# Kernel optimization log

Measured on AMD Instinct MI355X. Metric: run time of the kernel, lower is better.

## Reference

```python
import jax, jax.numpy as jnp
import numpy as np

B, S, E, H, L, V = 64, 512, 256, 256, 5, 50001  # vocab_size+1 rows, padding_idx=0
GC = 256  # gcn_hidden
NC = [10, 5]


def lstm_dir(x, Wih, Whh, b):
    # x: [B,S,D]; Wih: [4H,D]; Whh: [4H,H]; b: [4H] (= b_ih + b_hh)
    h0 = jnp.zeros((x.shape[0], Whh.shape[1]), x.dtype)
    def step(carry, xt):
        h, c = carry
        g = xt @ Wih.T + h @ Whh.T + b
        i, f, gg, o = jnp.split(g, 4, axis=-1)  # torch gate order i,f,g,o
        c = jax.nn.sigmoid(f) * c + jax.nn.sigmoid(i) * jnp.tanh(gg)
        h = jax.nn.sigmoid(o) * jnp.tanh(c)
        return (h, c), h
    _, hs = jax.lax.scan(step, (h0, h0), jnp.swapaxes(x, 0, 1))
    return jnp.swapaxes(hs, 0, 1)  # [B,S,H]


def layer_norm(x, g, b, eps=1e-5):
    mu = jnp.mean(x, -1, keepdims=True)
    var = jnp.mean((x - mu) ** 2, -1, keepdims=True)
    return (x - mu) * jax.lax.rsqrt(var + eps) * g + b


def banded_adj_matmul(x, mask):
    # adj has only super/sub-diagonal ones, masked by m_i*m_j, row-normalized (+1e-8).
    m = mask
    m_next = jnp.pad(m[:, 1:], ((0, 0), (0, 1)))
    m_prev = jnp.pad(m[:, :-1], ((0, 0), (1, 0)))
    rs = m * (m_prev + m_next) + 1e-8  # row sums
    c_next = (m * m_next / rs)[:, :, None]
    c_prev = (m * m_prev / rs)[:, :, None]
    x_next = jnp.pad(x[:, 1:], ((0, 0), (0, 1), (0, 0)))
    x_prev = jnp.pad(x[:, :-1], ((0, 0), (1, 0), (0, 0)))
    return c_next * x_next + c_prev * x_prev


def gcn_layer(x, mask, W, b, gamma, beta):
    h = banded_adj_matmul(x, mask)
    h = h @ W.T + b
    h = h + x  # in_dim == out_dim -> residual
    return jax.nn.relu(layer_norm(h, gamma, beta))


def setup_inputs() -> dict:
    key = jax.random.key(0)
    ks = jax.random.split(key, 24)
    rn = lambda k, sh, s=0.05: jax.random.normal(k, sh, jnp.float32) * s
    seq = jax.random.randint(ks[0], (B, S), 0, V, jnp.int32)
    mask = jnp.ones((B, S), jnp.float32)
    aux = rn(ks[1], (B, 6), 1.0)
    emb_table = rn(ks[2], (V, E), 0.1).at[0].set(0.0)  # padding_idx=0
    Wih0 = rn(ks[3], (2, 4 * H, E))
    Whh0 = rn(ks[4], (2, 4 * H, H))
    b0 = rn(ks[5], (2, 4 * H))
    Wih = rn(ks[6], (L - 1, 2, 4 * H, 2 * H))
    Whh = rn(ks[7], (L - 1, 2, 4 * H, H))
    bL = rn(ks[8], (L - 1, 2, 4 * H))
    gcn_W = rn(ks[9], (3, GC, E))
    gcn_b = rn(ks[10], (3, GC))
    gcn_gamma = jnp.ones((3, GC), jnp.float32)
    gcn_beta = jnp.zeros((3, GC), jnp.float32)
    fusion = 2 * H + GC + 6
    fc1_W = rn(ks[11], (512, fusion))
    fc1_b = rn(ks[12], (512,))
    fc2_W = rn(ks[13], (256, 512))
    fc2_b = rn(ks[14], (256,))
    head0_W = rn(ks[15], (NC[0], 256))
    head0_b = rn(ks[16], (NC[0],))
    head1_W = rn(ks[17], (NC[1], 256))
    head1_b = rn(ks[18], (NC[1],))
    return dict(seq=seq, mask=mask, aux=aux, emb_table=emb_table, Wih0=Wih0,
                Whh0=Whh0, b0=b0, Wih=Wih, Whh=Whh, bL=bL, gcn_W=gcn_W,
                gcn_b=gcn_b, gcn_gamma=gcn_gamma, gcn_beta=gcn_beta,
                fc1_W=fc1_W, fc1_b=fc1_b, fc2_W=fc2_W, fc2_b=fc2_b,
                head0_W=head0_W, head0_b=head0_b, head1_W=head1_W, head1_b=head1_b)


def reference(seq, mask, aux, emb_table, Wih0, Whh0, b0, Wih, Whh, bL,
              gcn_W, gcn_b, gcn_gamma, gcn_beta, fc1_W, fc1_b, fc2_W, fc2_b,
              head0_W, head0_b, head1_W, head1_b):
    emb = emb_table[seq]  # [B,S,E]; dropout = identity (eval)
    # 5-layer bidirectional LSTM
    out = emb
    for l in range(L):
        wih, whh, b = (Wih0, Whh0, b0) if l == 0 else (Wih[l - 1], Whh[l - 1], bL[l - 1])
        fwd = lstm_dir(out, wih[0], whh[0], b[0])
        bwd = jnp.flip(lstm_dir(jnp.flip(out, 1), wih[1], whh[1], b[1]), 1)
        out = jnp.concatenate([fwd, bwd], -1)  # [B,S,2H]
    lstm_out = out * mask[:, :, None]
    denom = jnp.clip(jnp.sum(mask, 1, keepdims=True), 1e-8)
    lstm_feat = jnp.sum(lstm_out, 1) / denom  # [B,2H]
    # GCN stack over banded adjacency
    g = emb
    for i in range(3):
        g = gcn_layer(g, mask, gcn_W[i], gcn_b[i], gcn_gamma[i], gcn_beta[i])
    g = g * mask[:, :, None]
    gcn_feat = jnp.sum(g, 1) / denom  # [B,GC]
    fused = jnp.concatenate([lstm_feat, gcn_feat, aux], 1)
    s = jax.nn.relu(fused @ fc1_W.T + fc1_b)
    s = jax.nn.relu(s @ fc2_W.T + fc2_b)
    return (s @ head0_W.T + head0_b, s @ head1_W.T + head1_b)
```

## Files before the change

kernel.cpp:

```cpp
#include <hip/hip_runtime.h>
#include <stdint.h>
#include <stddef.h>

typedef __bf16 bf16;
typedef __bf16 bf16x8 __attribute__((ext_vector_type(8)));
typedef __bf16 bf16x4 __attribute__((ext_vector_type(4)));
typedef float  f32x4  __attribute__((ext_vector_type(4)));
typedef int    v4i    __attribute__((ext_vector_type(4)));

#define NB   64
#define NS   512
#define NE   256
#define NH   256
#define NL   5
#define NGC  256
#define FUSION 774

__device__ __forceinline__ float sigm(float x) {
    return __fdividef(1.f, 1.f + __expf(-x));
}
__device__ __forceinline__ float tanh_(float x) {
    return __fdividef(2.f, 1.f + __expf(-2.f * x)) - 1.f;
}

__device__ __forceinline__ void gload_lds16(const void* g, void* l) {
    __builtin_amdgcn_global_load_lds(
        (const __attribute__((address_space(1))) void*)g,
        (__attribute__((address_space(3))) void*)l,
        16, 0, 0);
}

__global__ void k_cvt(const float* __restrict__ src, bf16* __restrict__ dst, int n4) {
    int i = blockIdx.x * 256 + threadIdx.x;
    if (i >= n4) return;
    f32x4 v = ((const f32x4*)src)[i];
    bf16x4 o;
    o[0] = (bf16)v[0]; o[1] = (bf16)v[1]; o[2] = (bf16)v[2]; o[3] = (bf16)v[3];
    ((bf16x4*)dst)[i] = o;
}

__global__ void k_cvt_perm(const float* __restrict__ src, bf16* __restrict__ dst,
                           int K, int nrows) {
    int r = blockIdx.x * 4 + (threadIdx.x >> 6);
    int lane = threadIdx.x & 63;
    if (r >= nrows) return;
    int g = r & 3, j = (r >> 2) & 255;
    int srcrow = (r & ~1023) | (g << 8) | j;
    const float* s = src + (size_t)srcrow * K;
    bf16* dp = dst + (size_t)r * K;
    for (int c = lane * 4; c < K; c += 256) {
        f32x4 v = *(const f32x4*)(s + c);
        bf16x4 o;
        o[0] = (bf16)v[0]; o[1] = (bf16)v[1]; o[2] = (bf16)v[2]; o[3] = (bf16)v[3];
        *(bf16x4*)(dp + c) = o;
    }
}

__global__ void k_perm_bias(const float* __restrict__ b0, const float* __restrict__ bL,
                            float* __restrict__ pb) {
    int i = blockIdx.x * 256 + threadIdx.x;
    int r = i & 2047;
    int layer = i >> 11;
    int g = r & 3, j = (r >> 2) & 255, dh = r >> 10;
    int srcidx = dh * 1024 + g * 256 + j;
    float v = (layer == 0) ? b0[srcidx] : bL[(size_t)(layer - 1) * 2048 + srcidx];
    pb[i] = v;
}

__global__ void k_embed(const int* __restrict__ seq, const float* __restrict__ table,
                        float* __restrict__ ef, bf16* __restrict__ eb) {
    int t  = blockIdx.x * 256 + threadIdx.x;
    int bs = t >> 6;
    int c4 = (t & 63) << 2;
    int row = seq[bs];
    f32x4 v = *(const f32x4*)(table + (size_t)row * NE + c4);
    *(f32x4*)(ef + (size_t)bs * NE + c4) = v;
    bf16x4 o;
    o[0] = (bf16)v[0]; o[1] = (bf16)v[1]; o[2] = (bf16)v[2]; o[3] = (bf16)v[3];
    *(bf16x4*)(eb + (size_t)bs * NE + c4) = o;
}

__global__ __launch_bounds__(256, 2)
void k_gemm(const bf16* __restrict__ A, const bf16* __restrict__ W,
            const float* __restrict__ bias, void* __restrict__ Cout,
            int M, int N, int K, int out_mode) {
    __shared__ __align__(16) bf16 sA[128 * 64];
    __shared__ __align__(16) bf16 sB[128 * 64];
    const int mblk = M >> 7;
    int bm = blockIdx.x % mblk;
    int bn = blockIdx.x / mblk;
    int m0 = bm << 7, n0 = bn << 7;
    int tid  = threadIdx.x;
    int wave = tid >> 6, lane = tid & 63;
    int wm = wave >> 1, wn = wave & 1;
    int l15 = lane & 15, quad = lane >> 4;

    f32x4 acc[4][4] = {};

    const int r0 = tid >> 3;
    const int c0 = (tid & 7) * 8;
    const bf16* Ab = A + (size_t)(m0 + r0) * K + c0;
    const bf16* Wb = W + (size_t)(n0 + r0) * K + c0;
    bf16* sAd = sA + tid * 8;
    bf16* sBd = sB + tid * 8;

    for (int k0 = 0; k0 < K; k0 += 64) {
#pragma unroll
        for (int i = 0; i < 4; i++) {
            gload_lds16(Ab + (size_t)(i * 32) * K + k0, sAd + i * 2048);
            gload_lds16(Wb + (size_t)(i * 32) * K + k0, sBd + i * 2048);
        }
        __syncthreads();
#pragma unroll
        for (int kk = 0; kk < 2; kk++) {
            bf16x8 af[4], bfr[4];
#pragma unroll
            for (int mt = 0; mt < 4; mt++)
                af[mt] = *(const bf16x8*)(sA + (wm * 64 + mt * 16 + l15) * 64 + kk * 32 + quad * 8);
#pragma unroll
            for (int nt = 0; nt < 4; nt++)
                bfr[nt] = *(const bf16x8*)(sB + (wn * 64 + nt * 16 + l15) * 64 + kk * 32 + quad * 8);
#pragma unroll
            for (int mt = 0; mt < 4; mt++)
#pragma unroll
                for (int nt = 0; nt < 4; nt++)
                    acc[mt][nt] = __builtin_amdgcn_mfma_f32_16x16x32_bf16(af[mt], bfr[nt], acc[mt][nt], 0, 0, 0);
        }
        __syncthreads();
    }
#pragma unroll
    for (int mt = 0; mt < 4; mt++) {
#pragma unroll
        for (int nt = 0; nt < 4; nt++) {
            int col = n0 + wn * 64 + nt * 16 + l15;
            float bv = bias[col];
            int row0 = m0 + wm * 64 + mt * 16 + quad * 4;
#pragma unroll
            for (int r4 = 0; r4 < 4; r4++) {
                float v = acc[mt][nt][r4] + bv;
                int r = row0 + r4;
                if (out_mode == 1) {
                    ((bf16*)Cout)[(size_t)r * N + col] = (bf16)v;
                } else {
                    ((float*)Cout)[(size_t)r * N + col] = v;
                }
            }
        }
    }
}

__global__ void k_prep_i8(const float* __restrict__ Whh0, const float* __restrict__ WhhL,
                          signed char* __restrict__ Wp8, float* __restrict__ scales) {
    int gw = blockIdx.x * 4 + (threadIdx.x >> 6);
    int lane = threadIdx.x & 63;
    int row = gw & 1023;
    int d = (gw >> 10) & 1;
    int layer = gw >> 11;
    const float* src = (layer == 0)
        ? (Whh0 + ((size_t)d * 1024 + row) * 256)
        : (WhhL + (((size_t)(layer - 1) * 2 + d) * 1024 + row) * 256);
    f32x4 v = *(const f32x4*)(src + lane * 4);
    float am = fmaxf(fmaxf(fabsf(v[0]), fabsf(v[1])), fmaxf(fabsf(v[2]), fabsf(v[3])));
#pragma unroll
    for (int off = 32; off >= 1; off >>= 1) am = fmaxf(am, __shfl_xor(am, off));
    am = fmaxf(am, 1e-8f);
    float inv = 127.f / am;
    int q0 = (int)__builtin_rintf(v[0] * inv);
    int q1 = (int)__builtin_rintf(v[1] * inv);
    int q2 = (int)__builtin_rintf(v[2] * inv);
    int q3 = (int)__builtin_rintf(v[3] * inv);
    uint32_t packed = (q0 & 255) | ((q1 & 255) << 8) | ((q2 & 255) << 16) | ((q3 & 255) << 24);
    int g = row >> 8, rem = row & 255;
    int w = rem >> 4, l15r = rem & 15;
    int k = lane * 4;
    int kt = k >> 6, q = (k >> 4) & 3, j = k & 15;
    size_t cell = ((size_t)layer * 2 + d) * 256 + (w * 4 + g) * 4 + kt;
    *(uint32_t*)(Wp8 + cell * 1024 + (q * 16 + l15r) * 16 + j) = packed;
    if (lane == 0)
        scales[((size_t)layer * 2 + d) * 1024 + row] = am * (1.f / (127.f * 127.f));
}

__global__ __launch_bounds__(512, 2)
void k_lstm_i8(const bf16* __restrict__ G,
               const signed char* __restrict__ Wp8,
               const float* __restrict__ sc,
               bf16* __restrict__ io_out)
{
    __shared__ signed char hs[2][2 * 4 * 80];

    const int d   = blockIdx.x & 1;
    const int bg  = blockIdx.x >> 1;
    const int tid = threadIdx.x;
    const int w = tid >> 6, lane = tid & 63;
    const int l15 = lane & 15, quad = lane >> 4;
    const int b_loc = quad & 1;
    const int jg    = quad >> 1;
    const int b = bg * 2 + b_loc;
    const int j = (w + jg * 8) * 16 + l15;

    v4i Wr[2][4][4];
#pragma unroll
    for (int sl = 0; sl < 2; sl++) {
        const int ws = w + sl * 8;
        const signed char* wb = Wp8 + ((size_t)d * 256 + ws * 16) * 1024 + lane * 16;
#pragma unroll
        for (int g = 0; g < 4; g++)
#pragma unroll
            for (int kt = 0; kt < 4; kt++)
                Wr[sl][g][kt] = *(const v4i*)(wb + (g * 4 + kt) * 1024);
    }
#pragma unroll
    for (int sl = 0; sl < 2; sl++)
#pragma unroll
        for (int g = 0; g < 4; g++)
#pragma unroll
            for (int kt = 0; kt < 4; kt++)
                asm volatile("" : "+v"(Wr[sl][g][kt]));

    float scv[4];
#pragma unroll
    for (int g = 0; g < 4; g++)
        scv[g] = sc[d * 1024 + g * 256 + j];

    const bf16* gbase = G + d * 1024 + j * 4;
    const size_t iob = (size_t)b * NS * 512 + d * 256 + j;

    const int hwr = (b_loc * 4 + (j >> 6)) * 80 + (j & 63);
    const int hrd = (((l15 >> 2) & 1) * 4 + (l15 & 3)) * 80 + quad * 16;
    const int rr = l15 & 3;

    float cst = 0.f;

    bf16x4 gcur = *(const bf16x4*)(gbase + (size_t)(b * 512 + (d ? (NS - 1) : 0)) * 2048);
    bf16x4 gnxt = *(const bf16x4*)(gbase + (size_t)(b * 512 + (d ? (NS - 2) : 1)) * 2048);

    {
        bf16x4 gfut = *(const bf16x4*)(gbase + (size_t)(b * 512 + (d ? (NS - 3) : 2)) * 2048);
        float pi = (float)gcur[0];
        float pg = (float)gcur[2], po = (float)gcur[3];
        float ig = sigm(pi), gc = tanh_(pg), og = sigm(po);
        float c = ig * gc;
        cst = c;
        float hh = og * tanh_(c);
        const int tcur = d ? (NS - 1) : 0;
        io_out[iob + (size_t)tcur * 512] = (bf16)hh;
        hs[0][hwr] = (signed char)(int)__builtin_rintf(hh * 127.f);
        gcur = gnxt; gnxt = gfut;
        asm volatile("s_waitcnt lgkmcnt(0)" ::: "memory");
        __builtin_amdgcn_s_barrier();
        asm volatile("" ::: "memory");
    }

    for (int t = 1; t < NS; t++) {
        const int rb = (t + 1) & 1, wbuf = t & 1;

        bf16x4 gfut = gcur;
        if (t + 2 < NS) {
            const int tt2 = d ? (NS - 3 - t) : (t + 2);
            gfut = *(const bf16x4*)(gbase + (size_t)(b * 512 + tt2) * 2048);
        }

        v4i acc[2][4] = {};
        {
            v4i chunk = *(const v4i*)&hs[rb][hrd];
            v4i a[4];
#pragma unroll
            for (int kt = 0; kt < 4; kt++) {
                a[kt][0] = (rr == kt) ? chunk[0] : 0;
                a[kt][1] = (rr == kt) ? chunk[1] : 0;
                a[kt][2] = (rr == kt) ? chunk[2] : 0;
                a[kt][3] = (rr == kt) ? chunk[3] : 0;
            }
#pragma unroll
            for (int sl = 0; sl < 2; sl++)
#pragma unroll
                for (int g = 0; g < 4; g++)
#pragma unroll
                    for (int kt = 0; kt < 4; kt++)
                        acc[sl][g] = __builtin_amdgcn_mfma_i32_16x16x64_i8(a[kt], Wr[sl][g][kt], acc[sl][g], 0, 0, 0);
        }

        int s[4];
#pragma unroll
        for (int g = 0; g < 4; g++) {
            int s0 = acc[0][g][0] + acc[0][g][1] + acc[0][g][2] + acc[0][g][3];
            int s1 = acc[1][g][0] + acc[1][g][1] + acc[1][g][2] + acc[1][g][3];
            s[g] = jg ? s1 : s0;
        }
        float pi = (float)s[0] * scv[0] + (float)gcur[0];
        float pf = (float)s[1] * scv[1] + (float)gcur[1];
        float pg = (float)s[2] * scv[2] + (float)gcur[2];
        float po = (float)s[3] * scv[3] + (float)gcur[3];
        float ig = sigm(pi), fg = sigm(pf), gc = tanh_(pg), og = sigm(po);
        float c = fg * cst + ig * gc;
        cst = c;
        float hh = og * tanh_(c);
        const int tcur = d ? (NS - 1 - t) : t;
        io_out[iob + (size_t)tcur * 512] = (bf16)hh;
        hs[wbuf][hwr] = (signed char)(int)__builtin_rintf(hh * 127.f);

        gcur = gnxt; gnxt = gfut;

        asm volatile("s_waitcnt lgkmcnt(0)" ::: "memory");
        __builtin_amdgcn_s_barrier();
        asm volatile("" ::: "memory");
    }
}

__global__ void k_banded(const float* __restrict__ x, const float* __restrict__ mask,
                         bf16* __restrict__ outb) {
    int t  = blockIdx.x * 256 + threadIdx.x;
    int bs = t >> 6;
    int c4 = (t & 63) << 2;
    int s = bs & (NS - 1);
    float m  = mask[bs];
    float mn = (s < NS - 1) ? mask[bs + 1] : 0.f;
    float mp = (s > 0)      ? mask[bs - 1] : 0.f;
    float rs = m * (mp + mn) + 1e-8f;
    float cn = m * mn / rs;
    float cp = m * mp / rs;
    f32x4 vn = {}, vp = {};
    if (s < NS - 1) vn = *(const f32x4*)(x + (size_t)(bs + 1) * NGC + c4);
    if (s > 0)      vp = *(const f32x4*)(x + (size_t)(bs - 1) * NGC + c4);
    bf16x4 o;
#pragma unroll
    for (int i = 0; i < 4; i++) o[i] = (bf16)(cn * vn[i] + cp * vp[i]);
    *(bf16x4*)(outb + (size_t)bs * NGC + c4) = o;
}

__global__ void k_gcnpost(const float* __restrict__ gemm_out, const float* __restrict__ x,
                          const float* __restrict__ gamma, const float* __restrict__ beta,
                          float* __restrict__ outx) {
    int row  = blockIdx.x * 4 + (threadIdx.x >> 6);
    int lane = threadIdx.x & 63;
    const float* h  = gemm_out + (size_t)row * NGC;
    const float* xr = x + (size_t)row * NGC;
    f32x4 hv = *(const f32x4*)(h + lane * 4);
    f32x4 xv = *(const f32x4*)(xr + lane * 4);
    f32x4 v;
#pragma unroll
    for (int i = 0; i < 4; i++) v[i] = hv[i] + xv[i];
    float sum = v[0] + v[1] + v[2] + v[3];
#pragma unroll
    for (int off = 32; off >= 1; off >>= 1) sum += __shfl_xor(sum, off);
    float mu = sum * (1.f / NGC);
    float sq = 0.f;
    f32x4 dv;
#pragma unroll
    for (int i = 0; i < 4; i++) { dv[i] = v[i] - mu; sq += dv[i] * dv[i]; }
#pragma unroll
    for (int off = 32; off >= 1; off >>= 1) sq += __shfl_xor(sq, off);
    float inv = rsqrtf(sq * (1.f / NGC) + 1e-5f);
    f32x4 o;
#pragma unroll
    for (int i = 0; i < 4; i++) {
        int c = lane * 4 + i;
        float y = dv[i] * inv * gamma[c] + beta[c];
        o[i] = fmaxf(y, 0.f);
    }
    *(f32x4*)(outx + (size_t)row * NGC + lane * 4) = o;
}

__global__ void k_pool_bf16(const bf16* __restrict__ src, const float* __restrict__ mask,
                            float* __restrict__ feat) {
    int b = blockIdx.x, f = threadIdx.x;
    float acc = 0.f, dm = 0.f;
    for (int t = 0; t < NS; t++) {
        float m = mask[b * NS + t];
        acc += m * (float)src[((size_t)b * NS + t) * 512 + f];
        dm += m;
    }
    feat[b * 512 + f] = acc / fmaxf(dm, 1e-8f);
}
__global__ void k_pool_f32(const float* __restrict__ src, const float* __restrict__ mask,
                           float* __restrict__ feat) {
    int b = blockIdx.x, f = threadIdx.x;
    float acc = 0.f, dm = 0.f;
    for (int t = 0; t < NS; t++) {
        float m = mask[b * NS + t];
        acc += m * src[((size_t)b * NS + t) * NGC + f];
        dm += m;
    }
    feat[b * NGC + f] = acc / fmaxf(dm, 1e-8f);
}

__global__ __launch_bounds__(512)
void k_head(const float* __restrict__ lfeat, const float* __restrict__ gfeat,
            const float* __restrict__ aux,
            const float* __restrict__ fc1W, const float* __restrict__ fc1b,
            const float* __restrict__ fc2W, const float* __restrict__ fc2b,
            const float* __restrict__ h0W, const float* __restrict__ h0b,
            const float* __restrict__ h1W, const float* __restrict__ h1b,
            float* __restrict__ out) {
    __shared__ float fused[FUSION];
    __shared__ float s1[512];
    __shared__ float s2[256];
    int m = blockIdx.x, tid = threadIdx.x;
    if (tid < 512) fused[tid] = lfeat[m * 512 + tid];
    if (tid < 256) fused[512 + tid] = gfeat[m * 256 + tid];
    if (tid < 6)   fused[768 + tid] = aux[m * 6 + tid];
    __syncthreads();
    {
        float a = fc1b[tid];
        const float* w = fc1W + (size_t)tid * FUSION;
        for (int k = 0; k < FUSION; k++) a += w[k] * fused[k];
        s1[tid] = fmaxf(a, 0.f);
    }
    __syncthreads();
    if (tid < 256) {
        float a = fc2b[tid];
        const float* w = fc2W + (size_t)tid * 512;
        for (int k = 0; k < 512; k++) a += w[k] * s1[k];
        s2[tid] = fmaxf(a, 0.f);
    }
    __syncthreads();
    if (tid < 15) {
        if (tid < 10) {
            float a = h0b[tid];
            const float* w = h0W + (size_t)tid * 256;
            for (int k = 0; k < 256; k++) a += w[k] * s2[k];
            out[m * 10 + tid] = a;
        } else {
            int n = tid - 10;
            float a = h1b[n];
            const float* w = h1W + (size_t)n * 256;
            for (int k = 0; k < 256; k++) a += w[k] * s2[k];
            out[640 + m * 5 + n] = a;
        }
    }
}

extern "C" void kernel_launch(void* const* d_in, const int* in_sizes, int n_in,
                              void* d_out, int out_size, void* d_ws, size_t ws_size,
                              hipStream_t stream) {
    const int*   seq   = (const int*)d_in[0];
    const float* mask  = (const float*)d_in[1];
    const float* aux   = (const float*)d_in[2];
    const float* table = (const float*)d_in[3];
    const float* Wih0  = (const float*)d_in[4];
    const float* Whh0  = (const float*)d_in[5];
    const float* b0    = (const float*)d_in[6];
    const float* WihL  = (const float*)d_in[7];
    const float* WhhL  = (const float*)d_in[8];
    const float* bL    = (const float*)d_in[9];
    const float* gcnW  = (const float*)d_in[10];
    const float* gcnb  = (const float*)d_in[11];
    const float* gcnG  = (const float*)d_in[12];
    const float* gcnBe = (const float*)d_in[13];
    const float* fc1W  = (const float*)d_in[14];
    const float* fc1b  = (const float*)d_in[15];
    const float* fc2W  = (const float*)d_in[16];
    const float* fc2b  = (const float*)d_in[17];
    const float* h0W   = (const float*)d_in[18];
    const float* h0b   = (const float*)d_in[19];
    const float* h1W   = (const float*)d_in[20];
    const float* h1b   = (const float*)d_in[21];
    float* outp = (float*)d_out;

    char* ws = (char*)d_ws;
    const size_t MROWS = (size_t)NB * NS;
    signed char* Wp8 = (signed char*)(ws + 0);
    float* wsc     = (float*)(ws + 2621440);
    bf16*  Wbf     = (bf16*) (ws + 2662400);
    bf16*  wb0     = Wbf;
    bf16*  wbL     = Wbf + 524288;
    bf16*  wgcn    = Wbf + 524288 + 4194304;
    bf16*  emb_b   = (bf16*) (ws + 33554432);
    bf16*  io0     = (bf16*) (ws + 50331648);
    bf16*  io1     = (bf16*) (ws + 83886080);
    char*  Greg    =          ws + 117440512;
    bf16*  G       = (bf16*)  Greg;
    float* lfeat   = (float*)(ws + 251658240);
    float* gfeat   = (float*)(ws + 251789312);
    float* pbias   = (float*)(ws + 251854848);
    float* gcnA  = (float*)(Greg + 0);
    float* gcnB_ = (float*)(Greg + 33554432);
    float* ggemm = (float*)(Greg + 67108864);
    bf16*  gtmp  = (bf16*) (Greg + 100663296);
    (void)ws_size; (void)n_in; (void)in_sizes; (void)out_size;

    k_cvt_perm<<<dim3(512),  dim3(256), 0, stream>>>(Wih0, wb0, 256, 2048);
    k_cvt_perm<<<dim3(2048), dim3(256), 0, stream>>>(WihL, wbL, 512, 8192);
    k_perm_bias<<<dim3(40), dim3(256), 0, stream>>>(b0, bL, pbias);
    k_cvt<<<dim3(192),  dim3(256), 0, stream>>>(gcnW, wgcn, 49152);
    k_prep_i8<<<dim3(2560), dim3(256), 0, stream>>>(Whh0, WhhL, Wp8, wsc);

    k_embed<<<dim3(8192), dim3(256), 0, stream>>>(seq, table, gcnA, emb_b);

    const float* xcur = gcnA;
    float* xnxt[3] = {gcnB_, gcnA, gcnB_};
    for (int i = 0; i < 3; i++) {
        k_banded<<<dim3(8192), dim3(256), 0, stream>>>(xcur, mask, gtmp);
        k_gemm<<<dim3((MROWS / 128) * (NGC / 128)), dim3(256), 0, stream>>>(
            gtmp, wgcn + (size_t)i * NGC * NGC, gcnb + i * NGC, ggemm,
            (int)MROWS, NGC, NGC, 0);
        k_gcnpost<<<dim3(8192), dim3(256), 0, stream>>>(
            ggemm, xcur, gcnG + i * NGC, gcnBe + i * NGC, xnxt[i]);
        xcur = xnxt[i];
    }
    k_pool_f32<<<dim3(NB), dim3(NGC), 0, stream>>>(xcur, mask, gfeat);

    const bf16* Xin = emb_b;
    int Kin = NE;
    bf16* ios[2] = {io0, io1};
    for (int l = 0; l < NL; l++) {
        const bf16* wih = l ? (wbL + (size_t)(l - 1) * 1048576) : wb0;
        k_gemm<<<dim3((MROWS / 128) * (2048 / 128)), dim3(256), 0, stream>>>(
            Xin, wih, pbias + (size_t)l * 2048, G, (int)MROWS, 2048, Kin, 1);
        bf16* lio = ios[l & 1];
        k_lstm_i8<<<dim3(64), dim3(512), 0, stream>>>(
            G, Wp8 + (size_t)l * 524288, wsc + (size_t)l * 2048, lio);
        Xin = lio;
        Kin = 512;
    }
    k_pool_bf16<<<dim3(NB), dim3(512), 0, stream>>>(ios[(NL - 1) & 1], mask, lfeat);

    k_head<<<dim3(NB), dim3(512), 0, stream>>>(
        lfeat, gfeat, aux, fc1W, fc1b, fc2W, fc2b, h0W, h0b, h1W, h1b, outp);
}
```

Before: 3.217 ms.

## Fuse GCN GEMM with residual and LayerNorm, add XCD-aware GEMM block mapping

Replaces the separate GCN GEMM and post-processing kernels with one kernel. Each block computes a full 128x256 output row tile, adds bias and the residual, and performs LayerNorm plus ReLU in registers using a shared-memory cross-wave reduction. This removes the fp32 intermediate round trip through global memory. The generic GEMM also remaps block IDs so that each XCD gets a contiguous range of M blocks, aiming at better L2 locality. The fused kernel computes variance as E[x^2]-mu^2, which is less numerically stable, and it uses more registers per thread.

```diff
diff --git a/kernel.cpp b/kernel.cpp
--- a/kernel.cpp
+++ b/kernel.cpp
@@ -86,9 +86,18 @@
             int M, int N, int K, int out_mode) {
     __shared__ __align__(16) bf16 sA[128 * 64];
     __shared__ __align__(16) bf16 sB[128 * 64];
-    const int mblk = M >> 7;
-    int bm = blockIdx.x % mblk;
-    int bn = blockIdx.x / mblk;
+    const int mblk = M >> 7, nblk = N >> 7;
+    int bid = blockIdx.x;
+    int bm, bn;
+    if ((mblk & 7) == 0) {
+        int xcd = bid & 7, r = bid >> 3;
+        int bmo = r / nblk;
+        bm = xcd * (mblk >> 3) + bmo;
+        bn = r - bmo * nblk;
+    } else {
+        bm = bid % mblk;
+        bn = bid / mblk;
+    }
     int m0 = bm << 7, n0 = bn << 7;
     int tid  = threadIdx.x;
     int wave = tid >> 6, lane = tid & 63;
@@ -147,6 +156,137 @@
             }
         }
     }
+}
+
+__global__ __launch_bounds__(256, 2)
+void k_gcn_fused(const bf16* __restrict__ A,
+                 const bf16* __restrict__ W,
+                 const float* __restrict__ bias,
+                 const float* __restrict__ x,
+                 const float* __restrict__ gamma, const float* __restrict__ beta,
+                 float* __restrict__ outx)
+{
+    __shared__ __align__(16) bf16 sA[128 * 64];
+    __shared__ __align__(16) bf16 sB[2][128 * 64];
+    __shared__ float lnred[2][128][2];
+    const int m0 = blockIdx.x << 7;
+    int tid = threadIdx.x;
+    int wave = tid >> 6, lane = tid & 63;
+    int wm = wave >> 1, wn = wave & 1;
+    int l15 = lane & 15, quad = lane >> 4;
+
+    f32x4 acc[2][4][4] = {};
+
+    const int r0 = tid >> 3;
+    const int c0 = (tid & 7) * 8;
+    const bf16* Ab = A + (size_t)(m0 + r0) * 256 + c0;
+    const bf16* Wb = W + (size_t)r0 * 256 + c0;
+    bf16* sAd = sA + tid * 8;
+
+    for (int k0 = 0; k0 < 256; k0 += 64) {
+#pragma unroll
+        for (int i = 0; i < 4; i++) {
+            gload_lds16(Ab + (size_t)(i * 32) * 256 + k0, sAd + i * 2048);
+            gload_lds16(Wb + (size_t)(i * 32) * 256 + k0, sB[0] + tid * 8 + i * 2048);
+            gload_lds16(Wb + (size_t)(128 + i * 32) * 256 + k0, sB[1] + tid * 8 + i * 2048);
+        }
+        __syncthreads();
+#pragma unroll
+        for (int kk = 0; kk < 2; kk++) {
+            bf16x8 af[4];
+#pragma unroll
+            for (int mt = 0; mt < 4; mt++)
+                af[mt] = *(const bf16x8*)(sA + (wm * 64 + mt * 16 + l15) * 64 + kk * 32 + quad * 8);
+#pragma unroll
+            for (int bn = 0; bn < 2; bn++) {
+                bf16x8 bfr[4];
+#pragma unroll
+                for (int nt = 0; nt < 4; nt++)
+                    bfr[nt] = *(const bf16x8*)(sB[bn] + (wn * 64 + nt * 16 + l15) * 64 + kk * 32 + quad * 8);
+#pragma unroll
+                for (int mt = 0; mt < 4; mt++)
+#pragma unroll
+                    for (int nt = 0; nt < 4; nt++)
+                        acc[bn][mt][nt] = __builtin_amdgcn_mfma_f32_16x16x32_bf16(af[mt], bfr[nt], acc[bn][mt][nt], 0, 0, 0);
+            }
+        }
+        __syncthreads();
+    }
+
+    float psum[4][4], psq[4][4];
+#pragma unroll
+    for (int mt = 0; mt < 4; mt++)
+#pragma unroll
+        for (int r4 = 0; r4 < 4; r4++) { psum[mt][r4] = 0.f; psq[mt][r4] = 0.f; }
+
+#pragma unroll
+    for (int bn = 0; bn < 2; bn++)
+#pragma unroll
+        for (int nt = 0; nt < 4; nt++) {
+            int col = bn * 128 + wn * 64 + nt * 16 + l15;
+            float bv = bias[col];
+#pragma unroll
+            for (int mt = 0; mt < 4; mt++) {
+                int row0 = m0 + wm * 64 + mt * 16 + quad * 4;
+#pragma unroll
+                for (int r4 = 0; r4 < 4; r4++) {
+                    float v = acc[bn][mt][nt][r4] + bv + x[(size_t)(row0 + r4) * 256 + col];
+                    acc[bn][mt][nt][r4] = v;
+                    psum[mt][r4] += v;
+                    psq[mt][r4]  += v * v;
+                }
+            }
+        }
+#pragma unroll
+    for (int mt = 0; mt < 4; mt++)
+#pragma unroll
+        for (int r4 = 0; r4 < 4; r4++) {
+#pragma unroll
+            for (int off = 8; off >= 1; off >>= 1) {
+                psum[mt][r4] += __shfl_xor(psum[mt][r4], off);
+                psq[mt][r4]  += __shfl_xor(psq[mt][r4], off);
+            }
+        }
+    if (l15 == 0) {
+#pragma unroll
+        for (int mt = 0; mt < 4; mt++)
+#pragma unroll
+            for (int r4 = 0; r4 < 4; r4++) {
+                int rl = wm * 64 + mt * 16 + quad * 4 + r4;
+                lnred[wn][rl][0] = psum[mt][r4];
+                lnred[wn][rl][1] = psq[mt][r4];
+            }
+    }
+    __syncthreads();
+#pragma unroll
+    for (int mt = 0; mt < 4; mt++) {
+        int rl0 = wm * 64 + mt * 16 + quad * 4;
+#pragma unroll
+        for (int r4 = 0; r4 < 4; r4++) {
+            float s  = lnred[0][rl0 + r4][0] + lnred[1][rl0 + r4][0];
+            float sq = lnred[0][rl0 + r4][1] + lnred[1][rl0 + r4][1];
+            float mu = s * (1.f / 256.f);
+            float var = sq * (1.f / 256.f) - mu * mu;
+            psum[mt][r4] = mu;
+            psq[mt][r4]  = rsqrtf(var + 1e-5f);
+        }
+    }
+#pragma unroll
+    for (int bn = 0; bn < 2; bn++)
+#pragma unroll
+        for (int nt = 0; nt < 4; nt++) {
+            int col = bn * 128 + wn * 64 + nt * 16 + l15;
+            float gv = gamma[col], bv2 = beta[col];
+#pragma unroll
+            for (int mt = 0; mt < 4; mt++) {
+                int row0 = m0 + wm * 64 + mt * 16 + quad * 4;
+#pragma unroll
+                for (int r4 = 0; r4 < 4; r4++) {
+                    float y = (acc[bn][mt][nt][r4] - psum[mt][r4]) * psq[mt][r4] * gv + bv2;
+                    outx[(size_t)(row0 + r4) * 256 + col] = fmaxf(y, 0.f);
+                }
+            }
+        }
 }
 
 __global__ void k_prep_i8(const float* __restrict__ Whh0, const float* __restrict__ WhhL,
@@ -326,39 +466,6 @@
 #pragma unroll
     for (int i = 0; i < 4; i++) o[i] = (bf16)(cn * vn[i] + cp * vp[i]);
     *(bf16x4*)(outb + (size_t)bs * NGC + c4) = o;
-}
-
-__global__ void k_gcnpost(const float* __restrict__ gemm_out, const float* __restrict__ x,
-                          const float* __restrict__ gamma, const float* __restrict__ beta,
-                          float* __restrict__ outx) {
-    int row  = blockIdx.x * 4 + (threadIdx.x >> 6);
-    int lane = threadIdx.x & 63;
-    const float* h  = gemm_out + (size_t)row * NGC;
-    const float* xr = x + (size_t)row * NGC;
-    f32x4 hv = *(const f32x4*)(h + lane * 4);
-    f32x4 xv = *(const f32x4*)(xr + lane * 4);
-    f32x4 v;
-#pragma unroll
-    for (int i = 0; i < 4; i++) v[i] = hv[i] + xv[i];
-    float sum = v[0] + v[1] + v[2] + v[3];
-#pragma unroll
-    for (int off = 32; off >= 1; off >>= 1) sum += __shfl_xor(sum, off);
-    float mu = sum * (1.f / NGC);
-    float sq = 0.f;
-    f32x4 dv;
-#pragma unroll
-    for (int i = 0; i < 4; i++) { dv[i] = v[i] - mu; sq += dv[i] * dv[i]; }
-#pragma unroll
-    for (int off = 32; off >= 1; off >>= 1) sq += __shfl_xor(sq, off);
-    float inv = rsqrtf(sq * (1.f / NGC) + 1e-5f);
-    f32x4 o;
-#pragma unroll
-    for (int i = 0; i < 4; i++) {
-        int c = lane * 4 + i;
-        float y = dv[i] * inv * gamma[c] + beta[c];
-        o[i] = fmaxf(y, 0.f);
-    }
-    *(f32x4*)(outx + (size_t)row * NGC + lane * 4) = o;
 }
 
 __global__ void k_pool_bf16(const bf16* __restrict__ src, const float* __restrict__ mask,
@@ -475,7 +582,6 @@
     float* pbias   = (float*)(ws + 251854848);
     float* gcnA  = (float*)(Greg + 0);
     float* gcnB_ = (float*)(Greg + 33554432);
-    float* ggemm = (float*)(Greg + 67108864);
     bf16*  gtmp  = (bf16*) (Greg + 100663296);
     (void)ws_size; (void)n_in; (void)in_sizes; (void)out_size;
 
@@ -491,11 +597,9 @@
     float* xnxt[3] = {gcnB_, gcnA, gcnB_};
     for (int i = 0; i < 3; i++) {
         k_banded<<<dim3(8192), dim3(256), 0, stream>>>(xcur, mask, gtmp);
-        k_gemm<<<dim3((MROWS / 128) * (NGC / 128)), dim3(256), 0, stream>>>(
-            gtmp, wgcn + (size_t)i * NGC * NGC, gcnb + i * NGC, ggemm,
-            (int)MROWS, NGC, NGC, 0);
-        k_gcnpost<<<dim3(8192), dim3(256), 0, stream>>>(
-            ggemm, xcur, gcnG + i * NGC, gcnBe + i * NGC, xnxt[i]);
+        k_gcn_fused<<<dim3(MROWS / 128), dim3(256), 0, stream>>>(
+            gtmp, wgcn + (size_t)i * NGC * NGC, gcnb + i * NGC, xcur,
+            gcnG + i * NGC, gcnBe + i * NGC, xnxt[i]);
         xcur = xnxt[i];
     }
     k_pool_f32<<<dim3(NB), dim3(NGC), 0, stream>>>(xcur, mask, gfeat);
```

New measurement: 3.170 ms. About the same (-1.5%).
